# Optimization experiments

Measured on AMD Instinct MI355X. Metric: run time of the kernel, lower is better.

Reference implementation:

```python
import jax, jax.numpy as jnp
import numpy as np

N = 50000
E = 640000
F_IN = 96
H1 = 128
H2 = 128
NUM_CLASSES = 256
NGRAM = 3
D1 = 32
L2_EPS = 1e-12


def _prop(xt, src, dst, ew):
    # weighted scatter-add aggregation: out[dst] += ew * xt[src]
    return jax.ops.segment_sum(ew[:, None] * xt[src], dst, num_segments=N)


def _digcn_layer(x, W_mi, W_mo, W_sk, b_mi, b_mo, b_si, b_so, C_in, C_out,
                 ei_in, ew_in, ei_out, ew_out):
    x_sk = x @ W_sk  # skip transform shared by in/out branches
    ic = (_prop(x @ W_mi, ei_in[0], ei_in[1], ew_in) + b_mi
          + _prop(x_sk, ei_in[0], ei_in[1], ew_in) + b_si)
    oc = (_prop(x @ W_mo, ei_out[0], ei_out[1], ew_out) + b_mo
          + _prop(x_sk, ei_out[0], ei_out[1], ew_out) + b_so)
    return C_in * ic + C_out * oc  # C_* are [N,1] vector coefficients


def setup_inputs() -> dict:
    key = jax.random.key(0)
    ks = jax.random.split(key, 32)
    s = 0.05
    d = {
        'x': jax.random.normal(ks[0], (N, F_IN), dtype=jnp.float32),
        'edge_index_in': jax.random.randint(ks[1], (2, E), 0, N, dtype=jnp.int32),
        'edge_weight_in': jax.random.uniform(ks[2], (E,), dtype=jnp.float32),
        'edge_index_out': jax.random.randint(ks[3], (2, E), 0, N, dtype=jnp.int32),
        'edge_weight_out': jax.random.uniform(ks[4], (E,), dtype=jnp.float32),
        'pe_table': jax.random.normal(ks[5], (NGRAM, D1), dtype=jnp.float32) * s,
    }
    dims = [(F_IN, H1), (H1, H1), (H1, H2)]
    ki = 6
    for li, (di, do) in enumerate(dims, start=1):
        d[f'W{li}_main_in'] = jax.random.normal(ks[ki], (di, do), dtype=jnp.float32) * s; ki += 1
        d[f'W{li}_main_out'] = jax.random.normal(ks[ki], (di, do), dtype=jnp.float32) * s; ki += 1
        d[f'W{li}_skip'] = jax.random.normal(ks[ki], (di, do), dtype=jnp.float32) * s; ki += 1
        d[f'b{li}_main_in'] = jax.random.normal(ks[ki], (do,), dtype=jnp.float32) * s; ki += 1
        d[f'b{li}_main_out'] = jax.random.normal(ks[ki], (do,), dtype=jnp.float32) * s; ki += 1
        d[f'b{li}_skip_in'] = jax.random.normal(ks[ki], (do,), dtype=jnp.float32) * s; ki += 1
        d[f'b{li}_skip_out'] = jax.random.normal(ks[ki], (do,), dtype=jnp.float32) * s; ki += 1
        d[f'C{li}_in'] = 1.0 + jax.random.normal(ks[ki], (N, 1), dtype=jnp.float32) * 0.02; ki += 1
        d[f'C{li}_out'] = 1.0 + jax.random.normal(ks[ki], (N, 1), dtype=jnp.float32) * 0.02; ki += 1
    k2 = jax.random.split(ks[ki], 4)
    d['res1_W'] = jax.random.normal(k2[0], (F_IN, H1), dtype=jnp.float32) * s
    d['res1_b'] = jax.random.normal(k2[1], (H1,), dtype=jnp.float32) * s
    d['dec_W'] = jax.random.normal(k2[2], (H2, NUM_CLASSES), dtype=jnp.float32) * s
    d['dec_b'] = jax.random.normal(k2[3], (NUM_CLASSES,), dtype=jnp.float32) * s
    return d


def reference(x, edge_index_in, edge_weight_in, edge_index_out, edge_weight_out, pe_table,
              W1_main_in, W1_main_out, W1_skip, b1_main_in, b1_main_out, b1_skip_in, b1_skip_out, C1_in, C1_out,
              W2_main_in, W2_main_out, W2_skip, b2_main_in, b2_main_out, b2_skip_in, b2_skip_out, C2_in, C2_out,
              W3_main_in, W3_main_out, W3_skip, b3_main_in, b3_main_out, b3_skip_in, b3_skip_out, C3_in, C3_out,
              res1_W, res1_b, dec_W, dec_b):
    # learnable positional encoding: x viewed as [N, ngram, d1] + pe[pos]
    x = (x.reshape(-1, NGRAM, D1) + pe_table[None]).reshape(-1, NGRAM * D1)

    h1 = _digcn_layer(x, W1_main_in, W1_main_out, W1_skip, b1_main_in, b1_main_out,
                      b1_skip_in, b1_skip_out, C1_in, C1_out,
                      edge_index_in, edge_weight_in, edge_index_out, edge_weight_out)
    h1 = jax.nn.relu(h1 + (x @ res1_W + res1_b))  # residual_proj_1 (96 -> 128)

    h2 = _digcn_layer(h1, W2_main_in, W2_main_out, W2_skip, b2_main_in, b2_main_out,
                      b2_skip_in, b2_skip_out, C2_in, C2_out,
                      edge_index_in, edge_weight_in, edge_index_out, edge_weight_out)
    h2 = jax.nn.relu(h2 + h1)  # identity residual (128 == 128)

    h3 = _digcn_layer(h2, W3_main_in, W3_main_out, W3_skip, b3_main_in, b3_main_out,
                      b3_skip_in, b3_skip_out, C3_in, C3_out,
                      edge_index_in, edge_weight_in, edge_index_out, edge_weight_out)
    h3 = h3 + h2  # residual_proj_3 is Identity (hidden1 == hidden2)

    norm = jnp.maximum(jnp.linalg.norm(h3, axis=1, keepdims=True), L2_EPS)
    emb = h3 / norm  # F.normalize, eps=1e-12
    logits = emb @ dec_W + dec_b
    return jax.nn.log_softmax(logits, axis=-1), emb
```

## Files before the change

### kernel.cpp

```cpp
#include <hip/hip_runtime.h>
#include <hip/hip_bf16.h>

typedef unsigned short ushort_t;
typedef __attribute__((ext_vector_type(8))) short bf16x8;
typedef __attribute__((ext_vector_type(4))) float f32x4;

__device__ __forceinline__ float bf2f(ushort_t u) {
    union { unsigned int i; float f; } v; v.i = ((unsigned int)u) << 16; return v.f;
}
__device__ __forceinline__ ushort_t f2bf(float f) {
    unsigned int u = __float_as_uint(f);
    unsigned int r = u + 0x7FFFu + ((u >> 16) & 1u);
    return (ushort_t)(r >> 16);
}
__device__ __forceinline__ float ldf(const void* p, size_t i, int isf) {
    return isf ? ((const float*)p)[i] : bf2f(((const ushort_t*)p)[i]);
}

__global__ void probe_dtype_k(const void* __restrict__ x, int* __restrict__ flag) {
    int t = threadIdx.x;
    const float* xf = (const float*)x;
    int bad = 0;
    for (int i = t; i < 2048; i += 256) {
        unsigned int u = __float_as_uint(xf[i]);
        unsigned int e = (u >> 23) & 0xFFu;
        if (e >= 0xC0u) bad = 1;
    }
    __shared__ int s_bad;
    if (t == 0) s_bad = 0;
    __syncthreads();
    if (bad) atomicOr(&s_bad, 1);
    __syncthreads();
    if (t == 0) flag[0] = s_bad ? 0 : 1;
}

__global__ void count_dst_k(const int* __restrict__ ei, int* __restrict__ cnt, int E) {
    int e = blockIdx.x * 256 + threadIdx.x;
    if (e < E) atomicAdd(&cnt[ei[E + e]], 1);
}

__global__ __launch_bounds__(256) void scan1_k(const int* __restrict__ cntA, const int* __restrict__ cntB,
                                               int* __restrict__ offA, int* __restrict__ offB,
                                               int* __restrict__ sums, int n, int nChunks) {
    int set = blockIdx.y;
    const int* cnt = set ? cntB : cntA;
    int* off = set ? offB : offA;
    __shared__ int s[256];
    int t = threadIdx.x;
    int idx = blockIdx.x * 1024 + t * 4;
    int v[4];
#pragma unroll
    for (int i = 0; i < 4; ++i) v[i] = (idx + i < n) ? cnt[idx + i] : 0;
    int tsum = v[0] + v[1] + v[2] + v[3];
    s[t] = tsum;
    __syncthreads();
    for (int d = 1; d < 256; d <<= 1) {
        int x = (t >= d) ? s[t - d] : 0;
        __syncthreads();
        s[t] += x;
        __syncthreads();
    }
    int run = s[t] - tsum;
    if (t == 255) sums[set * nChunks + blockIdx.x] = s[255];
#pragma unroll
    for (int i = 0; i < 4; ++i) { if (idx + i < n) off[idx + i] = run; run += v[i]; }
}

__global__ __launch_bounds__(256) void scan2_k(int* __restrict__ sums, int nChunks) {
    __shared__ int s[256];
    int t = threadIdx.x;
    for (int set = 0; set < 2; ++set) {
        int v = (t < nChunks) ? sums[set * nChunks + t] : 0;
        s[t] = v;
        __syncthreads();
        for (int d = 1; d < 256; d <<= 1) {
            int x = (t >= d) ? s[t - d] : 0;
            __syncthreads();
            s[t] += x;
            __syncthreads();
        }
        if (t < nChunks) sums[set * nChunks + t] = s[t] - v;
        __syncthreads();
    }
}

__global__ __launch_bounds__(256) void scan3_k(int* __restrict__ offA, int* __restrict__ offB,
                                               const int* __restrict__ sums, int n, int nChunks, int E) {
    int set = blockIdx.y;
    int* off = set ? offB : offA;
    int base = sums[set * nChunks + blockIdx.x];
    int idx = blockIdx.x * 1024 + threadIdx.x * 4;
#pragma unroll
    for (int i = 0; i < 4; ++i) { if (idx + i < n) off[idx + i] += base; }
    if (blockIdx.x == 0 && threadIdx.x == 0) off[n] = E;
}

__global__ void fill_csr_k(const int* __restrict__ ei, const void* __restrict__ ew,
                           const int* __restrict__ off, int* __restrict__ cur,
                           uint2* __restrict__ pairs, int E,
                           const int* __restrict__ flagp) {
    int isf = *flagp;
    int e = blockIdx.x * 256 + threadIdx.x;
    if (e >= E) return;
    int d = ei[E + e];
    int p = off[d] + atomicAdd(&cur[d], 1);
    pairs[p] = make_uint2((unsigned)ei[e], __float_as_uint(ldf(ew, e, isf)));
}

__global__ void prep_bandT_k(ushort_t* __restrict__ Wt, int K, int colOff,
                             const void* __restrict__ A, const void* __restrict__ B, int n,
                             const int* __restrict__ flagp) {
    int isf = *flagp;
    int i = blockIdx.x * 256 + threadIdx.x;
    if (i >= n) return;
    int k = i >> 7, c = i & 127;
    float v = ldf(A, (size_t)k * 128 + c, isf);
    if (B) v += ldf(B, (size_t)k * 128 + c, isf);
    Wt[(size_t)(colOff + c) * K + k] = f2bf(v);
}

__global__ void prep_decT_k(ushort_t* __restrict__ Wdt, const void* __restrict__ W,
                            const int* __restrict__ flagp) {
    int isf = *flagp;
    int i = blockIdx.x * 256 + threadIdx.x;
    int k = i >> 8, c = i & 255;
    Wdt[(size_t)c * 128 + k] = f2bf(ldf(W, (size_t)k * 256 + c, isf));
}

struct BiasJob { const void* a; const void* b; float* dst; int n; };
struct BiasJobs { BiasJob j[8]; };
__global__ void prep_bias_k(BiasJobs jobs, const int* __restrict__ flagp) {
    int isf = *flagp;
    BiasJob jb = jobs.j[blockIdx.x];
    int t = threadIdx.x;
    if (t < jb.n) {
        float v = ldf(jb.a, t, isf);
        if (jb.b) v += ldf(jb.b, t, isf);
        jb.dst[t] = v;
    }
}

template<int K, int DOUT>
__global__ __launch_bounds__(256) void gemm_mfma_k(
    const ushort_t* __restrict__ A, const ushort_t* __restrict__ Wt,
    ushort_t* __restrict__ Y, int M) {
    constexpr int NT = DOUT / 16;
    int tid = threadIdx.x;
    int wave = tid >> 6, lane = tid & 63;
    int q = lane >> 4, l15 = lane & 15;
    int arow = blockIdx.x * 64 + wave * 16 + l15;
    int rowc = arow < M ? arow : M - 1;
    f32x4 acc[NT];
#pragma unroll
    for (int t = 0; t < NT; ++t) acc[t] = (f32x4){0.f, 0.f, 0.f, 0.f};
#pragma unroll
    for (int kc = 0; kc < K; kc += 32) {
        bf16x8 a = *(const bf16x8*)(A + (size_t)rowc * K + kc + q * 8);
#pragma unroll
        for (int t = 0; t < NT; ++t) {
            bf16x8 b = *(const bf16x8*)(Wt + (size_t)(t * 16 + l15) * K + kc + q * 8);
            acc[t] = __builtin_amdgcn_mfma_f32_16x16x32_bf16(a, b, acc[t], 0, 0, 0);
        }
    }
    int outRowBase = blockIdx.x * 64 + wave * 16 + q * 4;
#pragma unroll
    for (int t = 0; t < NT; ++t) {
        int col = t * 16 + l15;
#pragma unroll
        for (int i = 0; i < 4; ++i) {
            int r = outRowBase + i;
            if (r < M) Y[(size_t)r * DOUT + col] = f2bf(acc[t][i]);
        }
    }
}

__global__ __launch_bounds__(256) void gemm_mfma_x_k(
    const void* __restrict__ X, const ushort_t* __restrict__ Wt,
    ushort_t* __restrict__ Y, int M, const void* __restrict__ pe,
    const int* __restrict__ flagp) {
    constexpr int K = 96, DOUT = 384, NT = DOUT / 16;
    __shared__ float pes[96];
    int isf = *flagp;
    int tid = threadIdx.x;
    if (tid < 96) pes[tid] = ldf(pe, tid, isf);
    __syncthreads();
    int wave = tid >> 6, lane = tid & 63;
    int q = lane >> 4, l15 = lane & 15;
    int arow = blockIdx.x * 64 + wave * 16 + l15;
    int rowc = arow < M ? arow : M - 1;
    f32x4 acc[NT];
#pragma unroll
    for (int t = 0; t < NT; ++t) acc[t] = (f32x4){0.f, 0.f, 0.f, 0.f};
#pragma unroll
    for (int kc = 0; kc < K; kc += 32) {
        float va[8];
        size_t base = (size_t)rowc * K + kc + q * 8;
        if (isf) {
            float4 u0 = *(const float4*)((const float*)X + base);
            float4 u1 = *(const float4*)((const float*)X + base + 4);
            va[0] = u0.x; va[1] = u0.y; va[2] = u0.z; va[3] = u0.w;
            va[4] = u1.x; va[5] = u1.y; va[6] = u1.z; va[7] = u1.w;
        } else {
            const ushort_t* xp = (const ushort_t*)X + base;
#pragma unroll
            for (int i = 0; i < 8; ++i) va[i] = bf2f(xp[i]);
        }
        bf16x8 a;
        short* ap = (short*)&a;
#pragma unroll
        for (int i = 0; i < 8; ++i) ap[i] = (short)f2bf(va[i] + pes[kc + q * 8 + i]);
#pragma unroll
        for (int t = 0; t < NT; ++t) {
            bf16x8 b = *(const bf16x8*)(Wt + (size_t)(t * 16 + l15) * K + kc + q * 8);
            acc[t] = __builtin_amdgcn_mfma_f32_16x16x32_bf16(a, b, acc[t], 0, 0, 0);
        }
    }
    int outRowBase = blockIdx.x * 64 + wave * 16 + q * 4;
#pragma unroll
    for (int t = 0; t < NT; ++t) {
        int col = t * 16 + l15;
#pragma unroll
        for (int i = 0; i < 4; ++i) {
            int r = outRowBase + i;
            if (r < M) Y[(size_t)r * DOUT + col] = f2bf(acc[t][i]);
        }
    }
}

__device__ __forceinline__ void accum8(float* acc, uint4 v, float w) {
    unsigned u[4] = {v.x, v.y, v.z, v.w};
#pragma unroll
    for (int i = 0; i < 4; ++i) {
        acc[2 * i]     = fmaf(w, __uint_as_float(u[i] << 16), acc[2 * i]);
        acc[2 * i + 1] = fmaf(w, __uint_as_float(u[i] & 0xFFFF0000u), acc[2 * i + 1]);
    }
}

__device__ __forceinline__ void gatherq(
    const uint2* __restrict__ pairs, const ushort_t* __restrict__ rowbase, int ldY,
    int e0, int e1, int qtr, float* acc) {
    int e = e0;
    for (; e + 8 <= e1; e += 8) {
        uint2 pa = pairs[e + qtr];
        uint2 pb = pairs[e + qtr + 4];
        uint4 va = *(const uint4*)(rowbase + (size_t)pa.x * ldY);
        uint4 vb = *(const uint4*)(rowbase + (size_t)pb.x * ldY);
        accum8(acc, va, __uint_as_float(pa.y));
        accum8(acc, vb, __uint_as_float(pb.y));
    }
    for (; e < e1; e += 4) {
        int ee = e + qtr;
        if (ee < e1) {
            uint2 p = pairs[ee];
            uint4 v = *(const uint4*)(rowbase + (size_t)p.x * ldY);
            accum8(acc, v, __uint_as_float(p.y));
        }
    }
}

__global__ __launch_bounds__(256) void prop_combine_k(
    const ushort_t* __restrict__ Y, int ldY,
    const int* __restrict__ offI, const uint2* __restrict__ prI,
    const int* __restrict__ offO, const uint2* __restrict__ prO,
    const void* __restrict__ Cin, const void* __restrict__ Cout,
    const float* __restrict__ bin, const float* __restrict__ bout,
    const ushort_t* __restrict__ res, int ldR, int colR, const float* __restrict__ res_b,
    ushort_t* __restrict__ H, int M, int relu, const int* __restrict__ flagp) {
    int isf = *flagp;
    int node = blockIdx.x * 4 + (threadIdx.x >> 6);
    int lane = threadIdx.x & 63;
    if (node >= M) return;
    int qtr = lane >> 4, li = lane & 15;
    float ai[8], ao[8];
#pragma unroll
    for (int k = 0; k < 8; ++k) { ai[k] = 0.f; ao[k] = 0.f; }
    gatherq(prI, Y + li * 8,       ldY, offI[node], offI[node + 1], qtr, ai);
    gatherq(prO, Y + 128 + li * 8, ldY, offO[node], offO[node + 1], qtr, ao);
#pragma unroll
    for (int k = 0; k < 8; ++k) {
        ai[k] += __shfl_xor(ai[k], 16, 64);
        ai[k] += __shfl_xor(ai[k], 32, 64);
        ao[k] += __shfl_xor(ao[k], 16, 64);
        ao[k] += __shfl_xor(ao[k], 32, 64);
    }
    int j = li * 8;
    float ci = ldf(Cin, node, isf), co = ldf(Cout, node, isf);
    uint4 rv = *(const uint4*)(res + (size_t)node * ldR + colR + j);
    float4 b0 = *(const float4*)(bin + j);
    float4 b1 = *(const float4*)(bin + j + 4);
    float4 c0 = *(const float4*)(bout + j);
    float4 c1 = *(const float4*)(bout + j + 4);
    float binv[8]  = {b0.x, b0.y, b0.z, b0.w, b1.x, b1.y, b1.z, b1.w};
    float boutv[8] = {c0.x, c0.y, c0.z, c0.w, c1.x, c1.y, c1.z, c1.w};
    float rbv[8] = {0.f, 0.f, 0.f, 0.f, 0.f, 0.f, 0.f, 0.f};
    if (res_b) {
        float4 r0 = *(const float4*)(res_b + j);
        float4 r1 = *(const float4*)(res_b + j + 4);
        rbv[0] = r0.x; rbv[1] = r0.y; rbv[2] = r0.z; rbv[3] = r0.w;
        rbv[4] = r1.x; rbv[5] = r1.y; rbv[6] = r1.z; rbv[7] = r1.w;
    }
    unsigned rw[4] = {rv.x, rv.y, rv.z, rv.w};
    float vo[8];
#pragma unroll
    for (int k = 0; k < 8; ++k) {
        float r = (k & 1) ? __uint_as_float(rw[k >> 1] & 0xFFFF0000u)
                          : __uint_as_float(rw[k >> 1] << 16);
        float v = ci * (ai[k] + binv[k]) + co * (ao[k] + boutv[k]) + r + rbv[k];
        if (relu) v = fmaxf(v, 0.f);
        vo[k] = v;
    }
    if (qtr == 0) {
        uint4 outv;
        unsigned* op = (unsigned*)&outv;
#pragma unroll
        for (int k = 0; k < 4; ++k)
            op[k] = ((unsigned)f2bf(vo[2 * k + 1]) << 16) | (unsigned)f2bf(vo[2 * k]);
        *(uint4*)(H + (size_t)node * 128 + j) = outv;
    }
}

__global__ __launch_bounds__(256) void decoder_mfma_k(
    const ushort_t* __restrict__ h3, const ushort_t* __restrict__ Wdt,
    const float* __restrict__ biasDec, void* __restrict__ d_out, int M,
    const int* __restrict__ flagp) {
    __shared__ ushort_t embLds[64 * 136];
    __shared__ float sb[256];
    int isf = *flagp;
    int tid = threadIdx.x;
    sb[tid] = biasDec[tid];
    int rowBase = blockIdx.x * 64;
    {
        int r = tid >> 2;
        int c0 = (tid & 3) * 32;
        int grow = rowBase + r;
        uint4 u[4] = {};
        if (grow < M) {
            const uint4* p = (const uint4*)(h3 + (size_t)grow * 128 + c0);
            u[0] = p[0]; u[1] = p[1]; u[2] = p[2]; u[3] = p[3];
        }
        float v[32];
#pragma unroll
        for (int b = 0; b < 4; ++b) {
            unsigned w[4] = {u[b].x, u[b].y, u[b].z, u[b].w};
#pragma unroll
            for (int i = 0; i < 4; ++i) {
                v[b * 8 + 2 * i]     = bf2f((ushort_t)(w[i] & 0xffffu));
                v[b * 8 + 2 * i + 1] = bf2f((ushort_t)(w[i] >> 16));
            }
        }
        float ss = 0.f;
#pragma unroll
        for (int i = 0; i < 32; ++i) ss += v[i] * v[i];
        ss += __shfl_xor(ss, 1, 64);
        ss += __shfl_xor(ss, 2, 64);
        float inv = 1.0f / fmaxf(sqrtf(ss), 1e-12f);
#pragma unroll
        for (int i = 0; i < 32; ++i) v[i] *= inv;
        unsigned* lp = (unsigned*)&embLds[r * 136 + c0];
#pragma unroll
        for (int i = 0; i < 16; ++i)
            lp[i] = ((unsigned)f2bf(v[2 * i + 1]) << 16) | (unsigned)f2bf(v[2 * i]);
        if (grow < M) {
            if (isf) {
                float* op = (float*)d_out + (size_t)M * 256 + (size_t)grow * 128 + c0;
#pragma unroll
                for (int i = 0; i < 32; ++i) op[i] = v[i];
            } else {
                unsigned* op = (unsigned*)((ushort_t*)d_out + (size_t)M * 256 + (size_t)grow * 128 + c0);
#pragma unroll
                for (int i = 0; i < 16; ++i)
                    op[i] = ((unsigned)f2bf(v[2 * i + 1]) << 16) | (unsigned)f2bf(v[2 * i]);
            }
        }
    }
    __syncthreads();
    int wave = tid >> 6, lane = tid & 63, q = lane >> 4, l15 = lane & 15;
    f32x4 acc[16];
#pragma unroll
    for (int t = 0; t < 16; ++t) acc[t] = (f32x4){0.f, 0.f, 0.f, 0.f};
    int ldsRow = wave * 16 + l15;
#pragma unroll
    for (int kc = 0; kc < 128; kc += 32) {
        bf16x8 a = *(const bf16x8*)(&embLds[ldsRow * 136 + kc + q * 8]);
#pragma unroll
        for (int t = 0; t < 16; ++t) {
            bf16x8 b = *(const bf16x8*)(Wdt + (size_t)(t * 16 + l15) * 128 + kc + q * 8);
            acc[t] = __builtin_amdgcn_mfma_f32_16x16x32_bf16(a, b, acc[t], 0, 0, 0);
        }
    }
#pragma unroll
    for (int t = 0; t < 16; ++t) {
        float b = sb[t * 16 + l15];
        acc[t][0] += b; acc[t][1] += b; acc[t][2] += b; acc[t][3] += b;
    }
#pragma unroll
    for (int i = 0; i < 4; ++i) {
        int grow = rowBase + wave * 16 + q * 4 + i;
        float mx = acc[0][i];
#pragma unroll
        for (int t = 1; t < 16; ++t) mx = fmaxf(mx, acc[t][i]);
        mx = fmaxf(mx, __shfl_xor(mx, 1, 64));
        mx = fmaxf(mx, __shfl_xor(mx, 2, 64));
        mx = fmaxf(mx, __shfl_xor(mx, 4, 64));
        mx = fmaxf(mx, __shfl_xor(mx, 8, 64));
        float sm = 0.f;
#pragma unroll
        for (int t = 0; t < 16; ++t) sm += __expf(acc[t][i] - mx);
        sm += __shfl_xor(sm, 1, 64);
        sm += __shfl_xor(sm, 2, 64);
        sm += __shfl_xor(sm, 4, 64);
        sm += __shfl_xor(sm, 8, 64);
        float offv = mx + __logf(sm);
        if (grow < M) {
            if (isf) {
                float* op = (float*)d_out + (size_t)grow * 256 + l15;
#pragma unroll
                for (int t = 0; t < 16; ++t) op[t * 16] = acc[t][i] - offv;
            } else {
                ushort_t* op = (ushort_t*)d_out + (size_t)grow * 256 + l15;
#pragma unroll
                for (int t = 0; t < 16; ++t) op[t * 16] = f2bf(acc[t][i] - offv);
            }
        }
    }
}

extern "C" void kernel_launch(void* const* d_in, const int* in_sizes, int n_in,
                              void* d_out, int out_size, void* d_ws, size_t ws_size,
                              hipStream_t stream) {
    const int N = in_sizes[0] / 96;
    const int E = in_sizes[2];

    const void* x      = d_in[0];
    const int*  ei_in  = (const int*)d_in[1];
    const void* ew_in  = d_in[2];
    const int*  ei_out = (const int*)d_in[3];
    const void* ew_out = d_in[4];
    const void* pe     = d_in[5];

    const void *W_mi[3], *W_mo[3], *W_sk[3], *b_mi[3], *b_mo[3], *b_si[3], *b_so[3], *C_i[3], *C_o[3];
    for (int l = 0; l < 3; ++l) {
        int base = 6 + l * 9;
        W_mi[l] = d_in[base + 0];
        W_mo[l] = d_in[base + 1];
        W_sk[l] = d_in[base + 2];
        b_mi[l] = d_in[base + 3];
        b_mo[l] = d_in[base + 4];
        b_si[l] = d_in[base + 5];
        b_so[l] = d_in[base + 6];
        C_i[l]  = d_in[base + 7];
        C_o[l]  = d_in[base + 8];
    }
    const void* res1_W = d_in[33];
    const void* res1_b = d_in[34];
    const void* dec_W  = d_in[35];
    const void* dec_b  = d_in[36];

    char* ws = (char*)d_ws;
    size_t off = 0;
    auto alloc = [&](size_t bytes) -> void* {
        void* p = ws + off;
        off = (off + bytes + 255) & ~(size_t)255;
        return p;
    };
    const int nChunks = (N + 1023) / 1024;
    int*   flag    = (int*)alloc(4);
    int*   off_in  = (int*)alloc((size_t)(N + 1) * 4);
    int*   cnt_in  = (int*)alloc((size_t)2 * N * 4);
    int*   cur_in  = cnt_in + N;
    uint2* pr_in   = (uint2*)alloc((size_t)E * 8);
    int*   off_out = (int*)alloc((size_t)(N + 1) * 4);
    int*   cnt_out = (int*)alloc((size_t)2 * N * 4);
    int*   cur_out = cnt_out + N;
    uint2* pr_out  = (uint2*)alloc((size_t)E * 8);
    int*   sums    = (int*)alloc((size_t)2 * nChunks * 4);
    ushort_t* Wt1  = (ushort_t*)alloc((size_t)384 * 96 * 2);
    ushort_t* Wt2  = (ushort_t*)alloc((size_t)256 * 128 * 2);
    ushort_t* Wt3  = (ushort_t*)alloc((size_t)256 * 128 * 2);
    ushort_t* Wdt  = (ushort_t*)alloc((size_t)256 * 128 * 2);
    float* biasBlk = (float*)alloc((size_t)1152 * 4);
    float* bin1 = biasBlk, *bout1 = biasBlk + 128, *bin2 = biasBlk + 256, *bout2 = biasBlk + 384;
    float* bin3 = biasBlk + 512, *bout3 = biasBlk + 640, *res1b = biasBlk + 768, *decb = biasBlk + 896;
    ushort_t* Yb  = (ushort_t*)alloc((size_t)N * 384 * 2);
    ushort_t* H1  = (ushort_t*)alloc((size_t)N * 128 * 2);
    ushort_t* H2  = (ushort_t*)alloc((size_t)N * 128 * 2);
    ushort_t* H3  = H1;

    probe_dtype_k<<<1, 256, 0, stream>>>(x, flag);

    hipMemsetAsync(cnt_in, 0, (size_t)2 * N * 4, stream);
    hipMemsetAsync(cnt_out, 0, (size_t)2 * N * 4, stream);
    int egrid = (E + 255) / 256;
    count_dst_k<<<egrid, 256, 0, stream>>>(ei_in, cnt_in, E);
    count_dst_k<<<egrid, 256, 0, stream>>>(ei_out, cnt_out, E);
    {
        dim3 g(nChunks, 2);
        scan1_k<<<g, 256, 0, stream>>>(cnt_in, cnt_out, off_in, off_out, sums, N, nChunks);
        scan2_k<<<1, 256, 0, stream>>>(sums, nChunks);
        scan3_k<<<g, 256, 0, stream>>>(off_in, off_out, sums, N, nChunks, E);
    }
    fill_csr_k<<<egrid, 256, 0, stream>>>(ei_in, ew_in, off_in, cur_in, pr_in, E, flag);
    fill_csr_k<<<egrid, 256, 0, stream>>>(ei_out, ew_out, off_out, cur_out, pr_out, E, flag);

    prep_bandT_k<<<48, 256, 0, stream>>>(Wt1, 96, 0,   W_mi[0], W_sk[0], 128 * 96, flag);
    prep_bandT_k<<<48, 256, 0, stream>>>(Wt1, 96, 128, W_mo[0], W_sk[0], 128 * 96, flag);
    prep_bandT_k<<<48, 256, 0, stream>>>(Wt1, 96, 256, res1_W, (const void*)nullptr, 128 * 96, flag);
    prep_bandT_k<<<64, 256, 0, stream>>>(Wt2, 128, 0,   W_mi[1], W_sk[1], 128 * 128, flag);
    prep_bandT_k<<<64, 256, 0, stream>>>(Wt2, 128, 128, W_mo[1], W_sk[1], 128 * 128, flag);
    prep_bandT_k<<<64, 256, 0, stream>>>(Wt3, 128, 0,   W_mi[2], W_sk[2], 128 * 128, flag);
    prep_bandT_k<<<64, 256, 0, stream>>>(Wt3, 128, 128, W_mo[2], W_sk[2], 128 * 128, flag);
    prep_decT_k<<<128, 256, 0, stream>>>(Wdt, dec_W, flag);
    {
        BiasJobs jb;
        jb.j[0] = {b_mi[0], b_si[0], bin1, 128};
        jb.j[1] = {b_mo[0], b_so[0], bout1, 128};
        jb.j[2] = {b_mi[1], b_si[1], bin2, 128};
        jb.j[3] = {b_mo[1], b_so[1], bout2, 128};
        jb.j[4] = {b_mi[2], b_si[2], bin3, 128};
        jb.j[5] = {b_mo[2], b_so[2], bout3, 128};
        jb.j[6] = {res1_b, nullptr, res1b, 128};
        jb.j[7] = {dec_b, nullptr, decb, 256};
        prep_bias_k<<<8, 256, 0, stream>>>(jb, flag);
    }

    int gBlocks = (N + 63) / 64;
    int pgrid = (N + 3) / 4;

    gemm_mfma_x_k<<<gBlocks, 256, 0, stream>>>(x, Wt1, Yb, N, pe, flag);
    prop_combine_k<<<pgrid, 256, 0, stream>>>(Yb, 384,
        off_in, pr_in, off_out, pr_out,
        C_i[0], C_o[0], bin1, bout1, Yb, 384, 256, res1b, H1, N, 1, flag);
    gemm_mfma_k<128, 256><<<gBlocks, 256, 0, stream>>>(H1, Wt2, Yb, N);
    prop_combine_k<<<pgrid, 256, 0, stream>>>(Yb, 256,
        off_in, pr_in, off_out, pr_out,
        C_i[1], C_o[1], bin2, bout2, H1, 128, 0, (const float*)nullptr, H2, N, 1, flag);
    gemm_mfma_k<128, 256><<<gBlocks, 256, 0, stream>>>(H2, Wt3, Yb, N);
    prop_combine_k<<<pgrid, 256, 0, stream>>>(Yb, 256,
        off_in, pr_in, off_out, pr_out,
        C_i[2], C_o[2], bin3, bout3, H2, 128, 0, (const float*)nullptr, H3, N, 0, flag);
    decoder_mfma_k<<<gBlocks, 256, 0, stream>>>(H3, Wdt, decb, d_out, N, flag);
}
```

Baseline: 653.1 us.

## Merge setup kernels and split prop gather across in/out halves

Fuses the dtype probe with the count zeroing, merges the in/out count and CSR fill kernels into single launches, and folds the eight weight-prep launches into one job-table kernel, cutting launch count. The propagation kernel now gives half of each wavefront to the in-edges and half to the out-edges, so both gathers run concurrently instead of back to back. The halves are then exchanged with shuffles. Idle lanes can appear when in/out degrees differ, because the loop runs to the longer of the two lists.

```diff
diff --git a/kernel.cpp b/kernel.cpp
--- a/kernel.cpp
+++ b/kernel.cpp
@@ -17,26 +17,37 @@
     return isf ? ((const float*)p)[i] : bf2f(((const ushort_t*)p)[i]);
 }
 
-__global__ void probe_dtype_k(const void* __restrict__ x, int* __restrict__ flag) {
-    int t = threadIdx.x;
-    const float* xf = (const float*)x;
-    int bad = 0;
-    for (int i = t; i < 2048; i += 256) {
-        unsigned int u = __float_as_uint(xf[i]);
-        unsigned int e = (u >> 23) & 0xFFu;
-        if (e >= 0xC0u) bad = 1;
-    }
-    __shared__ int s_bad;
-    if (t == 0) s_bad = 0;
-    __syncthreads();
-    if (bad) atomicOr(&s_bad, 1);
-    __syncthreads();
-    if (t == 0) flag[0] = s_bad ? 0 : 1;
-}
-
-__global__ void count_dst_k(const int* __restrict__ ei, int* __restrict__ cnt, int E) {
-    int e = blockIdx.x * 256 + threadIdx.x;
-    if (e < E) atomicAdd(&cnt[ei[E + e]], 1);
+__global__ void init_k(int* __restrict__ cntI, int* __restrict__ cntO, int n2,
+                       const void* __restrict__ x, int* __restrict__ flag) {
+    int i = blockIdx.x * 256 + threadIdx.x;
+    if (i < n2) { cntI[i] = 0; cntO[i] = 0; }
+    if (blockIdx.x == 0) {
+        int t = threadIdx.x;
+        const float* xf = (const float*)x;
+        int bad = 0;
+        for (int k = t; k < 2048; k += 256) {
+            unsigned int u = __float_as_uint(xf[k]);
+            unsigned int e = (u >> 23) & 0xFFu;
+            if (e >= 0xC0u) bad = 1;
+        }
+        __shared__ int s_bad;
+        if (t == 0) s_bad = 0;
+        __syncthreads();
+        if (bad) atomicOr(&s_bad, 1);
+        __syncthreads();
+        if (t == 0) flag[0] = s_bad ? 0 : 1;
+    }
+}
+
+__global__ void count_both_k(const int* __restrict__ eiI, const int* __restrict__ eiO,
+                             int* __restrict__ cntI, int* __restrict__ cntO,
+                             int E, int egrid) {
+    int set = blockIdx.x >= egrid ? 1 : 0;
+    int e = (blockIdx.x - set * egrid) * 256 + threadIdx.x;
+    if (e >= E) return;
+    const int* ei = set ? eiO : eiI;
+    int* cnt = set ? cntO : cntI;
+    atomicAdd(&cnt[ei[E + e]], 1);
 }
 
 __global__ __launch_bounds__(256) void scan1_k(const int* __restrict__ cntA, const int* __restrict__ cntB,
@@ -95,36 +106,43 @@
     if (blockIdx.x == 0 && threadIdx.x == 0) off[n] = E;
 }
 
-__global__ void fill_csr_k(const int* __restrict__ ei, const void* __restrict__ ew,
-                           const int* __restrict__ off, int* __restrict__ cur,
-                           uint2* __restrict__ pairs, int E,
-                           const int* __restrict__ flagp) {
+__global__ void fill_both_k(const int* __restrict__ eiI, const void* __restrict__ ewI,
+                            const int* __restrict__ eiO, const void* __restrict__ ewO,
+                            const int* __restrict__ offI, const int* __restrict__ offO,
+                            int* __restrict__ curI, int* __restrict__ curO,
+                            uint2* __restrict__ prI, uint2* __restrict__ prO,
+                            int E, int egrid, const int* __restrict__ flagp) {
     int isf = *flagp;
-    int e = blockIdx.x * 256 + threadIdx.x;
+    int set = blockIdx.x >= egrid ? 1 : 0;
+    int e = (blockIdx.x - set * egrid) * 256 + threadIdx.x;
     if (e >= E) return;
+    const int* ei = set ? eiO : eiI;
+    const void* ew = set ? ewO : ewI;
+    const int* off = set ? offO : offI;
+    int* cur = set ? curO : curI;
+    uint2* pr = set ? prO : prI;
     int d = ei[E + e];
     int p = off[d] + atomicAdd(&cur[d], 1);
-    pairs[p] = make_uint2((unsigned)ei[e], __float_as_uint(ldf(ew, e, isf)));
-}
-
-__global__ void prep_bandT_k(ushort_t* __restrict__ Wt, int K, int colOff,
-                             const void* __restrict__ A, const void* __restrict__ B, int n,
-                             const int* __restrict__ flagp) {
+    pr[p] = make_uint2((unsigned)ei[e], __float_as_uint(ldf(ew, e, isf)));
+}
+
+struct PrepJob { const void* A; const void* B; ushort_t* dst; int K; int colOff; int cshift; int n; int blkBase; };
+struct PrepJobsT { PrepJob j[8]; };
+__global__ __launch_bounds__(256) void prep_all_k(PrepJobsT jobs, const int* __restrict__ flagp) {
     int isf = *flagp;
-    int i = blockIdx.x * 256 + threadIdx.x;
-    if (i >= n) return;
-    int k = i >> 7, c = i & 127;
-    float v = ldf(A, (size_t)k * 128 + c, isf);
-    if (B) v += ldf(B, (size_t)k * 128 + c, isf);
-    Wt[(size_t)(colOff + c) * K + k] = f2bf(v);
-}
-
-__global__ void prep_decT_k(ushort_t* __restrict__ Wdt, const void* __restrict__ W,
-                            const int* __restrict__ flagp) {
-    int isf = *flagp;
-    int i = blockIdx.x * 256 + threadIdx.x;
-    int k = i >> 8, c = i & 255;
-    Wdt[(size_t)c * 128 + k] = f2bf(ldf(W, (size_t)k * 256 + c, isf));
+    int b = blockIdx.x;
+    int ji = 0;
+#pragma unroll
+    for (int t = 1; t < 8; ++t) if (b >= jobs.j[t].blkBase) ji = t;
+    PrepJob jb = jobs.j[ji];
+    int i = (b - jb.blkBase) * 256 + threadIdx.x;
+    if (i >= jb.n) return;
+    int cmask = (1 << jb.cshift) - 1;
+    int k = i >> jb.cshift, c = i & cmask;
+    int Cw = cmask + 1;
+    float v = ldf(jb.A, (size_t)k * Cw + c, isf);
+    if (jb.B) v += ldf(jb.B, (size_t)k * Cw + c, isf);
+    jb.dst[(size_t)(jb.colOff + c) * jb.K + k] = f2bf(v);
 }
 
 struct BiasJob { const void* a; const void* b; float* dst; int n; };
@@ -236,28 +254,6 @@
     }
 }
 
-__device__ __forceinline__ void gatherq(
-    const uint2* __restrict__ pairs, const ushort_t* __restrict__ rowbase, int ldY,
-    int e0, int e1, int qtr, float* acc) {
-    int e = e0;
-    for (; e + 8 <= e1; e += 8) {
-        uint2 pa = pairs[e + qtr];
-        uint2 pb = pairs[e + qtr + 4];
-        uint4 va = *(const uint4*)(rowbase + (size_t)pa.x * ldY);
-        uint4 vb = *(const uint4*)(rowbase + (size_t)pb.x * ldY);
-        accum8(acc, va, __uint_as_float(pa.y));
-        accum8(acc, vb, __uint_as_float(pb.y));
-    }
-    for (; e < e1; e += 4) {
-        int ee = e + qtr;
-        if (ee < e1) {
-            uint2 p = pairs[ee];
-            uint4 v = *(const uint4*)(rowbase + (size_t)p.x * ldY);
-            accum8(acc, v, __uint_as_float(p.y));
-        }
-    }
-}
-
 __global__ __launch_bounds__(256) void prop_combine_k(
     const ushort_t* __restrict__ Y, int ldY,
     const int* __restrict__ offI, const uint2* __restrict__ prI,
@@ -270,18 +266,35 @@
     int node = blockIdx.x * 4 + (threadIdx.x >> 6);
     int lane = threadIdx.x & 63;
     if (node >= M) return;
-    int qtr = lane >> 4, li = lane & 15;
-    float ai[8], ao[8];
-#pragma unroll
-    for (int k = 0; k < 8; ++k) { ai[k] = 0.f; ao[k] = 0.f; }
-    gatherq(prI, Y + li * 8,       ldY, offI[node], offI[node + 1], qtr, ai);
-    gatherq(prO, Y + 128 + li * 8, ldY, offO[node], offO[node + 1], qtr, ao);
+    int half = lane >> 5;
+    int subq = (lane >> 4) & 1;
+    int li   = lane & 15;
+    int eI0 = offI[node], eI1 = offI[node + 1];
+    int eO0 = offO[node], eO1 = offO[node + 1];
+    int e0 = half ? eO0 : eI0;
+    int e1 = half ? eO1 : eI1;
+    const uint2* pairs = half ? prO : prI;
+    const ushort_t* rowbase = Y + half * 128 + li * 8;
+    int lenMax = max(eI1 - eI0, eO1 - eO0);
+    float acc[8];
+#pragma unroll
+    for (int k = 0; k < 8; ++k) acc[k] = 0.f;
+    for (int it = 0; it < lenMax; it += 4) {
+        int eeA = e0 + it + subq;
+        int eeB = eeA + 2;
+        bool mA = eeA < e1, mB = eeB < e1;
+        uint2 pa, pb;
+        uint4 va, vb;
+        if (mA) { pa = pairs[eeA]; va = *(const uint4*)(rowbase + (size_t)pa.x * ldY); }
+        if (mB) { pb = pairs[eeB]; vb = *(const uint4*)(rowbase + (size_t)pb.x * ldY); }
+        if (mA) accum8(acc, va, __uint_as_float(pa.y));
+        if (mB) accum8(acc, vb, __uint_as_float(pb.y));
+    }
+    float other[8];
 #pragma unroll
     for (int k = 0; k < 8; ++k) {
-        ai[k] += __shfl_xor(ai[k], 16, 64);
-        ai[k] += __shfl_xor(ai[k], 32, 64);
-        ao[k] += __shfl_xor(ao[k], 16, 64);
-        ao[k] += __shfl_xor(ao[k], 32, 64);
+        acc[k] += __shfl_xor(acc[k], 16, 64);
+        other[k] = __shfl_xor(acc[k], 32, 64);
     }
     int j = li * 8;
     float ci = ldf(Cin, node, isf), co = ldf(Cout, node, isf);
@@ -303,13 +316,15 @@
     float vo[8];
 #pragma unroll
     for (int k = 0; k < 8; ++k) {
+        float aiv = half ? other[k] : acc[k];
+        float aov = half ? acc[k] : other[k];
         float r = (k & 1) ? __uint_as_float(rw[k >> 1] & 0xFFFF0000u)
                           : __uint_as_float(rw[k >> 1] << 16);
-        float v = ci * (ai[k] + binv[k]) + co * (ao[k] + boutv[k]) + r + rbv[k];
+        float v = ci * (aiv + binv[k]) + co * (aov + boutv[k]) + r + rbv[k];
         if (relu) v = fmaxf(v, 0.f);
         vo[k] = v;
     }
-    if (qtr == 0) {
+    if ((lane >> 4) == 0) {
         uint4 outv;
         unsigned* op = (unsigned*)&outv;
 #pragma unroll
@@ -486,30 +501,35 @@
     ushort_t* H2  = (ushort_t*)alloc((size_t)N * 128 * 2);
     ushort_t* H3  = H1;
 
-    probe_dtype_k<<<1, 256, 0, stream>>>(x, flag);
-
-    hipMemsetAsync(cnt_in, 0, (size_t)2 * N * 4, stream);
-    hipMemsetAsync(cnt_out, 0, (size_t)2 * N * 4, stream);
+    {
+        int n2 = 2 * N;
+        int g = (n2 + 255) / 256;
+        init_k<<<g, 256, 0, stream>>>(cnt_in, cnt_out, n2, x, flag);
+    }
+
     int egrid = (E + 255) / 256;
-    count_dst_k<<<egrid, 256, 0, stream>>>(ei_in, cnt_in, E);
-    count_dst_k<<<egrid, 256, 0, stream>>>(ei_out, cnt_out, E);
+    count_both_k<<<2 * egrid, 256, 0, stream>>>(ei_in, ei_out, cnt_in, cnt_out, E, egrid);
     {
         dim3 g(nChunks, 2);
         scan1_k<<<g, 256, 0, stream>>>(cnt_in, cnt_out, off_in, off_out, sums, N, nChunks);
         scan2_k<<<1, 256, 0, stream>>>(sums, nChunks);
         scan3_k<<<g, 256, 0, stream>>>(off_in, off_out, sums, N, nChunks, E);
     }
-    fill_csr_k<<<egrid, 256, 0, stream>>>(ei_in, ew_in, off_in, cur_in, pr_in, E, flag);
-    fill_csr_k<<<egrid, 256, 0, stream>>>(ei_out, ew_out, off_out, cur_out, pr_out, E, flag);
-
-    prep_bandT_k<<<48, 256, 0, stream>>>(Wt1, 96, 0,   W_mi[0], W_sk[0], 128 * 96, flag);
-    prep_bandT_k<<<48, 256, 0, stream>>>(Wt1, 96, 128, W_mo[0], W_sk[0], 128 * 96, flag);
-    prep_bandT_k<<<48, 256, 0, stream>>>(Wt1, 96, 256, res1_W, (const void*)nullptr, 128 * 96, flag);
-    prep_bandT_k<<<64, 256, 0, stream>>>(Wt2, 128, 0,   W_mi[1], W_sk[1], 128 * 128, flag);
-    prep_bandT_k<<<64, 256, 0, stream>>>(Wt2, 128, 128, W_mo[1], W_sk[1], 128 * 128, flag);
-    prep_bandT_k<<<64, 256, 0, stream>>>(Wt3, 128, 0,   W_mi[2], W_sk[2], 128 * 128, flag);
-    prep_bandT_k<<<64, 256, 0, stream>>>(Wt3, 128, 128, W_mo[2], W_sk[2], 128 * 128, flag);
-    prep_decT_k<<<128, 256, 0, stream>>>(Wdt, dec_W, flag);
+    fill_both_k<<<2 * egrid, 256, 0, stream>>>(ei_in, ew_in, ei_out, ew_out,
+        off_in, off_out, cur_in, cur_out, pr_in, pr_out, E, egrid, flag);
+
+    {
+        PrepJobsT pj;
+        pj.j[0] = {W_mi[0], W_sk[0], Wt1, 96, 0,   7, 128 * 96, 0};
+        pj.j[1] = {W_mo[0], W_sk[0], Wt1, 96, 128, 7, 128 * 96, 48};
+        pj.j[2] = {res1_W, nullptr,  Wt1, 96, 256, 7, 128 * 96, 96};
+        pj.j[3] = {W_mi[1], W_sk[1], Wt2, 128, 0,   7, 128 * 128, 144};
+        pj.j[4] = {W_mo[1], W_sk[1], Wt2, 128, 128, 7, 128 * 128, 208};
+        pj.j[5] = {W_mi[2], W_sk[2], Wt3, 128, 0,   7, 128 * 128, 272};
+        pj.j[6] = {W_mo[2], W_sk[2], Wt3, 128, 128, 7, 128 * 128, 336};
+        pj.j[7] = {dec_W, nullptr, Wdt, 128, 0, 8, 32768, 400};
+        prep_all_k<<<528, 256, 0, stream>>>(pj, flag);
+    }
     {
         BiasJobs jb;
         jb.j[0] = {b_mi[0], b_si[0], bin1, 128};
```

Result: no change. 643.2 us (-1.5%).
